# Kernel tuning notes

Measured on AMD Instinct MI355X. Metric: run time of the kernel, lower is better.

The kernel has to match this reference:

```python
import jax, jax.numpy as jnp
import numpy as np

IN_FEATURES = 512
OUT_FEATURES = 10
NEURONS_STRUCTURES = [64, 128, 256, 512]
REPETITIONS = 5
NUM_ACTIVATIONS = 4  # relu, tanh, sigmoid, gelu (exact erf, matching torch nn.GELU)
NUM_MODELS = NUM_ACTIVATIONS * REPETITIONS * len(NEURONS_STRUCTURES)  # 80
TOTAL_HIDDEN = sum(NEURONS_STRUCTURES) * REPETITIONS * NUM_ACTIVATIONS  # 19200
BATCH = 1024


def _build_neuron_model_id():
    # Mirrors ParallelMLPs.__init__ construction order:
    # for act -> for rep -> for structure: assign consecutive model ids
    ids = []
    m = 0
    for _act in range(NUM_ACTIVATIONS):
        for _rep in range(REPETITIONS):
            for n in NEURONS_STRUCTURES:
                ids += [m] * n
                m += 1
    return np.asarray(ids, dtype=np.int32)


def setup_inputs() -> dict:
    key = jax.random.key(0)
    k1, k2, k3, k4, k5 = jax.random.split(key, 5)
    x = jax.random.normal(k1, (BATCH, IN_FEATURES), dtype=jnp.float32)
    hidden_w = jax.random.normal(k2, (TOTAL_HIDDEN, IN_FEATURES), dtype=jnp.float32) * 0.05
    hidden_b = jax.random.normal(k3, (TOTAL_HIDDEN,), dtype=jnp.float32) * 0.05
    out_w = jax.random.normal(k4, (OUT_FEATURES, TOTAL_HIDDEN), dtype=jnp.float32) * 0.05
    out_b = jax.random.normal(k5, (NUM_MODELS, OUT_FEATURES), dtype=jnp.float32) * 0.05
    neuron_model_id = jnp.asarray(_build_neuron_model_id())
    return {"x": x, "hidden_w": hidden_w, "hidden_b": hidden_b,
            "out_w": out_w, "out_b": out_b, "neuron_model_id": neuron_model_id}


def reference(x, hidden_w, hidden_b, out_w, out_b, neuron_model_id):
    # Shared hidden linear: [B, H]
    h = x @ hidden_w.T + hidden_b
    # Per-block activations on equal contiguous chunks of the hidden dim
    split = TOTAL_HIDDEN // NUM_ACTIVATIONS
    acts = [jax.nn.relu, jnp.tanh, jax.nn.sigmoid,
            lambda t: jax.nn.gelu(t, approximate=False)]
    a = jnp.concatenate(
        [f(h[:, i * split:(i + 1) * split]) for i, f in enumerate(acts)], axis=1)
    # Ragged grouped out-projection: contrib[h, b, o] = a[b, h] * out_w[o, h]
    contrib = a.T[:, :, None] * out_w.T[:, None, :]  # [H, B, O]
    grouped = jax.ops.segment_sum(contrib, neuron_model_id,
                                  num_segments=NUM_MODELS)  # [M, B, O]
    return jnp.transpose(grouped, (1, 0, 2)) + out_b[None, :, :]  # [B, M, O]
```

## Files before the change

kernel.cpp:

```cpp
#include <hip/hip_runtime.h>
#include <hip/hip_bf16.h>
#include <cstdint>
#include <cstddef>


typedef unsigned short u16;
typedef unsigned int u32;
typedef __bf16 bf16x8 __attribute__((ext_vector_type(8)));
typedef float f32x4 __attribute__((ext_vector_type(4)));

__device__ __forceinline__ u16 f2bf(float f) {
  u32 u = __builtin_bit_cast(u32, f);
  u += 0x7fffu + ((u >> 16) & 1u);
  return (u16)(u >> 16);
}
__device__ __forceinline__ float bf2f(u16 s) {
  u32 u = ((u32)s) << 16;
  return __builtin_bit_cast(float, u);
}

__device__ __forceinline__ void async16(void* l, const void* g) {
  __builtin_amdgcn_global_load_lds(
      (__attribute__((address_space(1))) void*)(void*)g,
      (__attribute__((address_space(3))) void*)l, 16, 0, 0);
}

__global__ __launch_bounds__(256) void cvt_kernel(
    const float4* __restrict__ xs, uint2* __restrict__ xd, int nx4,
    const float4* __restrict__ ws, uint2* __restrict__ wd, int nw4) {
  int i = blockIdx.x * blockDim.x + threadIdx.x;
  if (i >= nx4 + nw4) return;
  const float4* s; uint2* d; int j;
  if (i < nx4) { s = xs; d = xd; j = i; }
  else         { s = ws; d = wd; j = i - nx4; }
  float4 f = s[j];
  uint2 o;
  o.x = (u32)f2bf(f.x) | ((u32)f2bf(f.y) << 16);
  o.y = (u32)f2bf(f.z) | ((u32)f2bf(f.w) << 16);
  d[j] = o;
}

__global__ __launch_bounds__(256, 2) void gemm_act_kernel(
    const u16* __restrict__ A,
    const u16* __restrict__ Bw,
    const float* __restrict__ hbias,
    u16* __restrict__ aout) {
  __shared__ char lds[65536];
  const int t = threadIdx.x;
  const int lane = t & 63;
  const int w = t >> 6;
  const int bx = blockIdx.x % 150;
  const int by = blockIdx.x / 150;
  const int row0 = by * 128;
  const int col0 = bx * 128;
  const int wr = w >> 1, wc = w & 1;

  f32x4 acc[4][4];
#pragma unroll
  for (int m = 0; m < 4; ++m)
#pragma unroll
    for (int n = 0; n < 4; ++n)
#pragma unroll
      for (int r = 0; r < 4; ++r) acc[m][n][r] = 0.f;

  const int srow = t >> 3;
  const int sc8 = t & 7;

  auto stage = [&](int buf, int kt) {
    const int k0 = kt * 64;
#pragma unroll
    for (int i = 0; i < 4; ++i) {
      int row = i * 32 + srow;
      int c8 = sc8 ^ (row & 7);
      const u16* gA = A + (size_t)(row0 + row) * 512 + k0 + c8 * 8;
      const u16* gB = Bw + (size_t)(col0 + row) * 512 + k0 + c8 * 8;
      char* lA = lds + buf * 16384 + i * 4096 + w * 1024;
      char* lB = lds + 32768 + buf * 16384 + i * 4096 + w * 1024;
      async16(lA, gA);
      async16(lB, gB);
    }
  };

  auto compute = [&](int buf) {
    const char* baseA = lds + buf * 16384;
    const char* baseB = lds + 32768 + buf * 16384;
    const int il = lane & 15;
    const int kb0 = (lane >> 4) * 16;
#pragma unroll
    for (int ks = 0; ks < 2; ++ks) {
      bf16x8 av[4], bv[4];
#pragma unroll
      for (int m = 0; m < 4; ++m) {
        int row = wr * 64 + m * 16 + il;
        int off = row * 128 + ((ks * 64 + kb0) ^ ((row & 7) << 4));
        av[m] = *(const bf16x8*)(baseA + off);
      }
#pragma unroll
      for (int n = 0; n < 4; ++n) {
        int row = wc * 64 + n * 16 + il;
        int off = row * 128 + ((ks * 64 + kb0) ^ ((row & 7) << 4));
        bv[n] = *(const bf16x8*)(baseB + off);
      }
#pragma unroll
      for (int m = 0; m < 4; ++m)
#pragma unroll
        for (int n = 0; n < 4; ++n)
          acc[m][n] = __builtin_amdgcn_mfma_f32_16x16x32_bf16(av[m], bv[n],
                                                              acc[m][n], 0, 0, 0);
    }
  };

  stage(0, 0);
  __syncthreads();
#pragma unroll 2
  for (int kt = 0; kt < 8; ++kt) {
    int cur = kt & 1;
    if (kt < 7) stage(cur ^ 1, kt + 1);
    compute(cur);
    __syncthreads();
  }

  const int il = lane & 15;
  const int q = lane >> 4;
#pragma unroll
  for (int n = 0; n < 4; ++n) {
    int gcol = col0 + wc * 64 + n * 16 + il;
    int act = gcol / 4800;
    float bias = hbias[gcol];
#pragma unroll
    for (int m = 0; m < 4; ++m) {
      int growb = row0 + wr * 64 + m * 16 + q * 4;
#pragma unroll
      for (int r = 0; r < 4; ++r) {
        float v = acc[m][n][r] + bias;
        float o;
        if (act == 0)      o = fmaxf(v, 0.f);
        else if (act == 1) o = tanhf(v);
        else if (act == 2) o = 1.f / (1.f + __expf(-v));
        else               o = 0.5f * v * (1.f + erff(v * 0.70710678118f));
        aout[(size_t)(growb + r) * 19200 + gcol] = f2bf(o);
      }
    }
  }
}

__global__ __launch_bounds__(256) void layer2_kernel(
    const u16* __restrict__ a,
    const float* __restrict__ ow,
    const float* __restrict__ ob,
    float* __restrict__ out) {
  const int t = threadIdx.x;
  const int wid = blockIdx.x * 4 + (t >> 6);
  const int lane = t & 63;
  const int m = wid >> 8;
  const int btile = wid & 255;
  const int g = lane >> 4;
  const int il = lane & 15;
  const int b = btile * 4 + g;
  const int s = m & 3;
  const int r5 = (m >> 2) % 5;
  const int act = m / 20;
  const int start = act * 4800 + r5 * 960 + 64 * ((1 << s) - 1);
  const int len = 64 << s;

  const u16* arow = a + (size_t)b * 19200 + start;
  float acc[10];
#pragma unroll
  for (int o = 0; o < 10; ++o) acc[o] = 0.f;

  for (int j = il; j < len; j += 16) {
    float av = bf2f(arow[j]);
    int col = start + j;
#pragma unroll
    for (int o = 0; o < 10; ++o)
      acc[o] = fmaf(av, ow[o * 19200 + col], acc[o]);
  }
#pragma unroll
  for (int o = 0; o < 10; ++o) {
    float v = acc[o];
    v += __shfl_xor(v, 1);
    v += __shfl_xor(v, 2);
    v += __shfl_xor(v, 4);
    v += __shfl_xor(v, 8);
    acc[o] = v;
  }
  if (il < 10) {
    float res = 0.f;
#pragma unroll
    for (int o = 0; o < 10; ++o)
      if (il == o) res = acc[o];
    out[(size_t)b * 800 + m * 10 + il] = res + ob[m * 10 + il];
  }
}

extern "C" void kernel_launch(void* const* d_in, const int* in_sizes, int n_in,
                              void* d_out, int out_size, void* d_ws, size_t ws_size,
                              hipStream_t stream) {
  const float* x = (const float*)d_in[0];
  const float* hw = (const float*)d_in[1];
  const float* hb = (const float*)d_in[2];
  const float* ow = (const float*)d_in[3];
  const float* ob = (const float*)d_in[4];
  float* out = (float*)d_out;

  char* ws = (char*)d_ws;
  u16* xb = (u16*)ws;
  u16* wb = (u16*)(ws + 1048576);
  u16* ab = (u16*)(ws + 1048576 + 19660800);

  const int nx4 = (1024 * 512) / 4;
  const int nw4 = (19200 * 512) / 4;
  const int tot = nx4 + nw4;
  cvt_kernel<<<tot / 256, 256, 0, stream>>>((const float4*)x, (uint2*)xb, nx4,
                                            (const float4*)hw, (uint2*)wb, nw4);
  gemm_act_kernel<<<1200, 256, 0, stream>>>(xb, wb, hb, ab);
  layer2_kernel<<<5120, 256, 0, stream>>>(ab, ow, ob, out);
}
```

Baseline: 181.5 us.

## Use MFMA for layer-2 projection, remap GEMM tiles per XCD, drop LDS swizzle

```diff
diff --git a/kernel.cpp b/kernel.cpp
--- a/kernel.cpp
+++ b/kernel.cpp
@@ -14,15 +14,15 @@
   u += 0x7fffu + ((u >> 16) & 1u);
   return (u16)(u >> 16);
 }
-__device__ __forceinline__ float bf2f(u16 s) {
-  u32 u = ((u32)s) << 16;
-  return __builtin_bit_cast(float, u);
-}
 
 __device__ __forceinline__ void async16(void* l, const void* g) {
   __builtin_amdgcn_global_load_lds(
       (__attribute__((address_space(1))) void*)(void*)g,
       (__attribute__((address_space(3))) void*)l, 16, 0, 0);
+}
+
+__device__ __forceinline__ void drain_vm() {
+  asm volatile("s_waitcnt vmcnt(0)" ::: "memory");
 }
 
 __global__ __launch_bounds__(256) void cvt_kernel(
@@ -49,8 +49,10 @@
   const int t = threadIdx.x;
   const int lane = t & 63;
   const int w = t >> 6;
-  const int bx = blockIdx.x % 150;
-  const int by = blockIdx.x / 150;
+  const int c = blockIdx.x & 7;
+  const int L = c * 150 + (blockIdx.x >> 3);
+  const int bx = L >> 3;
+  const int by = L & 7;
   const int row0 = by * 128;
   const int col0 = bx * 128;
   const int wr = w >> 1, wc = w & 1;
@@ -67,40 +69,31 @@
   const int sc8 = t & 7;
 
   auto stage = [&](int buf, int kt) {
-    const int k0 = kt * 64;
+    const int k0 = kt * 64 + sc8 * 8;
 #pragma unroll
     for (int i = 0; i < 4; ++i) {
       int row = i * 32 + srow;
-      int c8 = sc8 ^ (row & 7);
-      const u16* gA = A + (size_t)(row0 + row) * 512 + k0 + c8 * 8;
-      const u16* gB = Bw + (size_t)(col0 + row) * 512 + k0 + c8 * 8;
-      char* lA = lds + buf * 16384 + i * 4096 + w * 1024;
-      char* lB = lds + 32768 + buf * 16384 + i * 4096 + w * 1024;
-      async16(lA, gA);
-      async16(lB, gB);
+      async16(lds + buf * 16384 + i * 4096 + w * 1024,
+              A + (size_t)(row0 + row) * 512 + k0);
+      async16(lds + 32768 + buf * 16384 + i * 4096 + w * 1024,
+              Bw + (size_t)(col0 + row) * 512 + k0);
     }
   };
 
+  const int il = lane & 15, q = lane >> 4;
+
   auto compute = [&](int buf) {
-    const char* baseA = lds + buf * 16384;
-    const char* baseB = lds + 32768 + buf * 16384;
-    const int il = lane & 15;
-    const int kb0 = (lane >> 4) * 16;
+    const char* bA = lds + buf * 16384;
+    const char* bB = lds + 32768 + buf * 16384;
 #pragma unroll
     for (int ks = 0; ks < 2; ++ks) {
       bf16x8 av[4], bv[4];
 #pragma unroll
-      for (int m = 0; m < 4; ++m) {
-        int row = wr * 64 + m * 16 + il;
-        int off = row * 128 + ((ks * 64 + kb0) ^ ((row & 7) << 4));
-        av[m] = *(const bf16x8*)(baseA + off);
-      }
-#pragma unroll
-      for (int n = 0; n < 4; ++n) {
-        int row = wc * 64 + n * 16 + il;
-        int off = row * 128 + ((ks * 64 + kb0) ^ ((row & 7) << 4));
-        bv[n] = *(const bf16x8*)(baseB + off);
-      }
+      for (int m = 0; m < 4; ++m)
+        av[m] = *(const bf16x8*)(bA + (wr * 64 + m * 16 + il) * 128 + ks * 64 + q * 16);
+#pragma unroll
+      for (int n = 0; n < 4; ++n)
+        bv[n] = *(const bf16x8*)(bB + (wc * 64 + n * 16 + il) * 128 + ks * 64 + q * 16);
 #pragma unroll
       for (int m = 0; m < 4; ++m)
 #pragma unroll
@@ -111,17 +104,16 @@
   };
 
   stage(0, 0);
+  drain_vm();
   __syncthreads();
-#pragma unroll 2
   for (int kt = 0; kt < 8; ++kt) {
     int cur = kt & 1;
     if (kt < 7) stage(cur ^ 1, kt + 1);
     compute(cur);
+    drain_vm();
     __syncthreads();
   }
 
-  const int il = lane & 15;
-  const int q = lane >> 4;
 #pragma unroll
   for (int n = 0; n < 4; ++n) {
     int gcol = col0 + wc * 64 + n * 16 + il;
@@ -150,46 +142,45 @@
     const float* __restrict__ ob,
     float* __restrict__ out) {
   const int t = threadIdx.x;
-  const int wid = blockIdx.x * 4 + (t >> 6);
   const int lane = t & 63;
-  const int m = wid >> 8;
-  const int btile = wid & 255;
-  const int g = lane >> 4;
-  const int il = lane & 15;
-  const int b = btile * 4 + g;
+  const int w = t >> 6;
+  const int m = blockIdx.x % 80;
+  const int bt = blockIdx.x / 80;
+  const int b0 = bt * 64 + w * 16;
   const int s = m & 3;
-  const int r5 = (m >> 2) % 5;
+  const int rep = (m >> 2) % 5;
   const int act = m / 20;
-  const int start = act * 4800 + r5 * 960 + 64 * ((1 << s) - 1);
-  const int len = 64 << s;
-
-  const u16* arow = a + (size_t)b * 19200 + start;
-  float acc[10];
-#pragma unroll
-  for (int o = 0; o < 10; ++o) acc[o] = 0.f;
-
-  for (int j = il; j < len; j += 16) {
-    float av = bf2f(arow[j]);
-    int col = start + j;
-#pragma unroll
-    for (int o = 0; o < 10; ++o)
-      acc[o] = fmaf(av, ow[o * 19200 + col], acc[o]);
-  }
-#pragma unroll
-  for (int o = 0; o < 10; ++o) {
-    float v = acc[o];
-    v += __shfl_xor(v, 1);
-    v += __shfl_xor(v, 2);
-    v += __shfl_xor(v, 4);
-    v += __shfl_xor(v, 8);
-    acc[o] = v;
-  }
+  const int seg0 = act * 4800 + rep * 960 + 64 * ((1 << s) - 1);
+  const int K = 64 << s;
+  const int il = lane & 15, q = lane >> 4;
+
+  f32x4 acc = {0.f, 0.f, 0.f, 0.f};
+  const u16* arow = a + (size_t)(b0 + il) * 19200 + seg0 + q * 8;
+  const float* wrow = ow + il * 19200 + seg0 + q * 8;
+  const bool wvalid = il < 10;
+
+  for (int k0 = 0; k0 < K; k0 += 32) {
+    bf16x8 af = *(const bf16x8*)(arow + k0);
+    union { bf16x8 v; u16 u[8]; } bb;
+    if (wvalid) {
+      float4 f0 = *(const float4*)(wrow + k0);
+      float4 f1 = *(const float4*)(wrow + k0 + 4);
+      bb.u[0] = f2bf(f0.x); bb.u[1] = f2bf(f0.y);
+      bb.u[2] = f2bf(f0.z); bb.u[3] = f2bf(f0.w);
+      bb.u[4] = f2bf(f1.x); bb.u[5] = f2bf(f1.y);
+      bb.u[6] = f2bf(f1.z); bb.u[7] = f2bf(f1.w);
+    } else {
+#pragma unroll
+      for (int j = 0; j < 8; ++j) bb.u[j] = 0;
+    }
+    acc = __builtin_amdgcn_mfma_f32_16x16x32_bf16(af, bb.v, acc, 0, 0, 0);
+  }
+
   if (il < 10) {
-    float res = 0.f;
-#pragma unroll
-    for (int o = 0; o < 10; ++o)
-      if (il == o) res = acc[o];
-    out[(size_t)b * 800 + m * 10 + il] = res + ob[m * 10 + il];
+    float bias = ob[m * 10 + il];
+#pragma unroll
+    for (int r = 0; r < 4; ++r)
+      out[(size_t)(b0 + q * 4 + r) * 800 + m * 10 + il] = acc[r] + bias;
   }
 }
 
@@ -214,5 +205,5 @@
   cvt_kernel<<<tot / 256, 256, 0, stream>>>((const float4*)x, (uint2*)xb, nx4,
                                             (const float4*)hw, (uint2*)wb, nw4);
   gemm_act_kernel<<<1200, 256, 0, stream>>>(xb, wb, hb, ab);
-  layer2_kernel<<<5120, 256, 0, stream>>>(ab, ow, ob, out);
-}
+  layer2_kernel<<<1280, 256, 0, stream>>>(ab, ow, ob, out);
+}
```

After: 182.6 us. About the same (+0.6%).
